# Performance work log

Hardware: AMD Instinct MI355X
Metric: run time of the kernel (lower is better)

## Reference

```python
import jax, jax.numpy as jnp
import numpy as np

NUM_HEADS = 8
NUM_POINTS = 4


def setup_inputs() -> dict:
    key = jax.random.key(0)
    bs, h, w = 2, 128, 128
    cin = cout = 256
    nq = h * w
    ks = jax.random.split(key, 6)
    query = jax.random.normal(ks[0], (bs, nq, cin), jnp.float32)
    value = jax.random.normal(ks[1], (bs, nq, cin), jnp.float32)
    # sampling_offsets: small random weight, bias = directional grid init (as in init_weights)
    W_off = jax.random.normal(ks[2], (cin, NUM_HEADS * NUM_POINTS * 2), jnp.float32) * 0.01
    thetas = np.arange(NUM_HEADS, dtype=np.float32) * (2.0 * np.pi / NUM_HEADS)
    grid = np.stack([np.cos(thetas), np.sin(thetas)], -1)
    grid = grid / np.abs(grid).max(-1, keepdims=True)
    grid = np.tile(grid[:, None, :], (1, NUM_POINTS, 1)) * (np.arange(NUM_POINTS, dtype=np.float32)[None, :, None] + 1.0)
    b_off = jnp.asarray(grid.reshape(-1), jnp.float32)
    W_attn = jax.random.normal(ks[3], (cin, NUM_HEADS * NUM_POINTS), jnp.float32) * 0.01
    b_attn = jnp.zeros((NUM_HEADS * NUM_POINTS,), jnp.float32)
    s = 1.0 / np.sqrt(cin)  # xavier-ish uniform
    W_val = jax.random.uniform(ks[4], (cin, cout), jnp.float32, -s, s)
    b_val = jnp.zeros((cout,), jnp.float32)
    W_out = jax.random.uniform(ks[5], (cout, cout), jnp.float32, -s, s)
    b_out = jnp.zeros((cout,), jnp.float32)
    return {"query": query, "value": value, "W_off": W_off, "b_off": b_off,
            "W_attn": W_attn, "b_attn": b_attn, "W_val": W_val, "b_val": b_val,
            "W_out": W_out, "b_out": b_out, "h": h, "w": w}


def _bilinear_sample(v_flat, ix, iy, h, w):
    # v_flat: (bs, heads, h*w, d); ix/iy: (bs, heads, nq, P) pixel coords.
    # grid_sample bilinear, align_corners=False, padding_mode='zeros'.
    x0 = jnp.floor(ix)
    y0 = jnp.floor(iy)
    wx1 = ix - x0
    wy1 = iy - y0
    bs, hd, nq, P = ix.shape
    acc = 0.0
    corners = ((x0, y0, (1.0 - wx1) * (1.0 - wy1)),
               (x0 + 1.0, y0, wx1 * (1.0 - wy1)),
               (x0, y0 + 1.0, (1.0 - wx1) * wy1),
               (x0 + 1.0, y0 + 1.0, wx1 * wy1))
    for xc, yc, wgt in corners:
        xi = xc.astype(jnp.int32)
        yi = yc.astype(jnp.int32)
        valid = (xi >= 0) & (xi < w) & (yi >= 0) & (yi < h)
        idx = jnp.clip(yi, 0, h - 1) * w + jnp.clip(xi, 0, w - 1)
        g = jnp.take_along_axis(v_flat, idx.reshape(bs, hd, nq * P)[..., None], axis=2)
        acc = acc + g.reshape(bs, hd, nq, P, -1) * (wgt * valid)[..., None]
    return acc  # (bs, heads, nq, P, d)


def deform_attn(query, value, W_off, b_off, W_attn, b_attn, W_val, b_val, h, w):
    bs, nq, _ = query.shape
    d = W_val.shape[1] // NUM_HEADS
    v = (value @ W_val + b_val).reshape(bs, nq, NUM_HEADS, d)
    off = (query @ W_off + b_off).reshape(bs, nq, NUM_HEADS, NUM_POINTS, 2)
    aw = jax.nn.softmax((query @ W_attn + b_attn).reshape(bs, nq, NUM_HEADS, NUM_POINTS), axis=-1)
    # reference points in [0,1], scale_ratio=1.0, (x, y) order
    ys = (jnp.arange(h, dtype=jnp.float32) + 0.5) / h
    xs = (jnp.arange(w, dtype=jnp.float32) + 0.5) / w
    ry, rx = jnp.meshgrid(ys, xs, indexing='ij')
    ref = jnp.stack([rx.reshape(-1), ry.reshape(-1)], -1)  # (nq, 2)
    loc = ref[None, :, None, None, :] + off / jnp.array([w, h], jnp.float32)
    grid = 2.0 * loc - 1.0  # normalized grid_sample coords
    grid = grid.transpose(0, 2, 1, 3, 4)  # (bs, heads, nq, P, 2)
    ix = (grid[..., 0] + 1.0) * (w / 2.0) - 0.5
    iy = (grid[..., 1] + 1.0) * (h / 2.0) - 0.5
    v_flat = v.transpose(0, 2, 1, 3)  # (bs, heads, h*w, d)
    sampled = _bilinear_sample(v_flat, ix, iy, h, w)  # (bs, heads, nq, P, d)
    out = (sampled * aw.transpose(0, 2, 1, 3)[..., None]).sum(3)  # (bs, heads, nq, d)
    return out.transpose(0, 2, 1, 3).reshape(bs, nq, NUM_HEADS * d)


def reference(query, value, W_off, b_off, W_attn, b_attn, W_val, b_val, W_out, b_out, h, w):
    attn = deform_attn(query, value, W_off, b_off, W_attn, b_attn, W_val, b_val, h, w)
    # dropout acts as identity in eval mode; identity residual = query
    return attn @ W_out + b_out + query
```

## Files before the change

### kernel.cpp

```cpp
#include <hip/hip_runtime.h>

#define H_IMG 128
#define W_IMG 128
#define NQ (H_IMG * W_IMG)
#define CIN 256
#define NH 8
#define NP 4
#define DH 32
#define LDSP 264

typedef __bf16 bf16x4 __attribute__((ext_vector_type(4)));
typedef __bf16 bf16x8 __attribute__((ext_vector_type(8)));
typedef _Float16 f16x8 __attribute__((ext_vector_type(8)));
typedef float f32x4 __attribute__((ext_vector_type(4)));

__global__ __launch_bounds__(256) void prep_weights(
    const float* __restrict__ Wval, const float* __restrict__ Wout,
    const float* __restrict__ Woff, const float* __restrict__ Wattn,
    const float* __restrict__ boff, const float* __restrict__ battn,
    __bf16* __restrict__ btv, _Float16* __restrict__ bto,
    __bf16* __restrict__ btoa, float* __restrict__ bias96) {
  int id = blockIdx.x * 256 + threadIdx.x;
  if (id < 256 * 256) {
    int n = id >> 8, k = id & 255;
    btv[n * 256 + k] = (__bf16)Wval[k * 256 + n];
    bto[n * 256 + k] = (_Float16)Wout[k * 256 + n];
  }
  if (id < 96 * 256) {
    int n = id >> 8, k = id & 255;
    float w = (n < 64) ? Woff[k * 64 + n] : Wattn[k * 32 + (n - 64)];
    btoa[n * 256 + k] = (__bf16)w;
  }
  if (id < 96) {
    bias96[id] = (id < 64) ? boff[id] : battn[id - 64];
  }
}

__global__ __launch_bounds__(512, 8) void gemm_v(
    const float* __restrict__ A, const __bf16* __restrict__ BT,
    const float* __restrict__ bias, _Float16* __restrict__ v, int M) {
  const int t = threadIdx.x;
  const int lane = t & 63;
  const int wave = t >> 6;
  const int r = lane & 15;
  const int q = lane >> 4;
  const int b = blockIdx.x;
  const int gm0 = (b & 511) * 64;
  const int wn = (b >> 9) * 128 + wave * 16;

  __shared__ __bf16 As[64 * LDSP];

#pragma unroll
  for (int i = 0; i < 8; ++i) {
    int g = i * 512 + t;
    int row = g >> 6, c4 = g & 63;
    float4 f = *(const float4*)(A + (size_t)(gm0 + row) * 256 + c4 * 4);
    bf16x4 hh;
    hh[0] = (__bf16)f.x; hh[1] = (__bf16)f.y;
    hh[2] = (__bf16)f.z; hh[3] = (__bf16)f.w;
    *(bf16x4*)(&As[row * LDSP + c4 * 4]) = hh;
  }
  __syncthreads();

  f32x4 acc[4];
#pragma unroll
  for (int mt = 0; mt < 4; ++mt) acc[mt] = (f32x4){0.f, 0.f, 0.f, 0.f};

#pragma unroll
  for (int kt = 0; kt < 8; ++kt) {
    const int ko = kt * 32 + q * 8;
    bf16x8 a[4];
#pragma unroll
    for (int mt = 0; mt < 4; ++mt)
      a[mt] = *(const bf16x8*)(&As[(mt * 16 + r) * LDSP + ko]);
    bf16x8 bb = *(const bf16x8*)(BT + (size_t)(wn + r) * 256 + ko);
#pragma unroll
    for (int mt = 0; mt < 4; ++mt)
      acc[mt] = __builtin_amdgcn_mfma_f32_16x16x32_bf16(a[mt], bb, acc[mt], 0, 0, 0);
  }

#pragma unroll
  for (int mt = 0; mt < 4; ++mt)
#pragma unroll
    for (int rr = 0; rr < 4; ++rr) {
      int row = gm0 + mt * 16 + q * 4 + rr;
      int col = wn + r;
      v[((size_t)(col >> 5) * M + row) * 32 + (col & 31)] =
          (_Float16)(acc[mt][rr] + bias[col]);
    }
}

__global__ __launch_bounds__(256, 2) void oa_sample_out(
    const float* __restrict__ query, const __bf16* __restrict__ btoa,
    const float* __restrict__ bias96, const _Float16* __restrict__ v,
    const _Float16* __restrict__ bto, const float* __restrict__ b_out,
    float* __restrict__ out, int M) {
  const int t = threadIdx.x;
  const int lane = t & 63;
  const int wave = t >> 6;
  const int r = lane & 15;
  const int q = lane >> 4;
  const int gm0 = blockIdx.x * 64;

  __shared__ __bf16 As[64 * LDSP];
  __shared__ float oas[64 * 100];
  _Float16* Asf = (_Float16*)As;

#pragma unroll
  for (int i = 0; i < 16; ++i) {
    int g = i * 256 + t;
    int row = g >> 6, c4 = g & 63;
    float4 f = *(const float4*)(query + (size_t)(gm0 + row) * 256 + c4 * 4);
    bf16x4 hh;
    hh[0] = (__bf16)f.x; hh[1] = (__bf16)f.y;
    hh[2] = (__bf16)f.z; hh[3] = (__bf16)f.w;
    *(bf16x4*)(&As[row * LDSP + c4 * 4]) = hh;
  }

  float resid[4][4][4];
#pragma unroll
  for (int mt = 0; mt < 4; ++mt)
#pragma unroll
    for (int nt = 0; nt < 4; ++nt)
#pragma unroll
      for (int rr = 0; rr < 4; ++rr)
        resid[mt][nt][rr] =
            query[(size_t)(gm0 + mt * 16 + q * 4 + rr) * 256 + wave * 64 + nt * 16 + r];

  __syncthreads();

  {
    const int wm = (wave & 1) * 32;
    const int n0 = (wave >> 1) * 48;
    f32x4 acc[2][3];
#pragma unroll
    for (int mt = 0; mt < 2; ++mt)
#pragma unroll
      for (int nt = 0; nt < 3; ++nt) acc[mt][nt] = (f32x4){0.f, 0.f, 0.f, 0.f};
#pragma unroll
    for (int kt = 0; kt < 8; ++kt) {
      const int ko = kt * 32 + q * 8;
      bf16x8 a0 = *(const bf16x8*)(&As[(wm + r) * LDSP + ko]);
      bf16x8 a1 = *(const bf16x8*)(&As[(wm + 16 + r) * LDSP + ko]);
      bf16x8 b[3];
#pragma unroll
      for (int nt = 0; nt < 3; ++nt)
        b[nt] = *(const bf16x8*)(btoa + (size_t)(n0 + nt * 16 + r) * 256 + ko);
#pragma unroll
      for (int nt = 0; nt < 3; ++nt) {
        acc[0][nt] = __builtin_amdgcn_mfma_f32_16x16x32_bf16(a0, b[nt], acc[0][nt], 0, 0, 0);
        acc[1][nt] = __builtin_amdgcn_mfma_f32_16x16x32_bf16(a1, b[nt], acc[1][nt], 0, 0, 0);
      }
    }
#pragma unroll
    for (int mt = 0; mt < 2; ++mt)
#pragma unroll
      for (int nt = 0; nt < 3; ++nt)
#pragma unroll
        for (int rr = 0; rr < 4; ++rr) {
          int rl = wm + mt * 16 + q * 4 + rr;
          int col = n0 + nt * 16 + r;
          oas[rl * 100 + col] = acc[mt][nt][rr] + bias96[col];
        }
  }
  __syncthreads();

  {
    const int qrow = t >> 2;
    const int c8 = (t & 3) * 8;
    const int row = gm0 + qrow;
    const int b = row >> 14;
    const int qi = row & (NQ - 1);
    const int x = qi & (W_IMG - 1);
    const int y = qi >> 7;
    const float* oar = &oas[qrow * 100];
#pragma unroll
    for (int h = 0; h < NH; ++h) {
      float l0 = oar[64 + h * 4 + 0];
      float l1 = oar[64 + h * 4 + 1];
      float l2 = oar[64 + h * 4 + 2];
      float l3 = oar[64 + h * 4 + 3];
      float mx = fmaxf(fmaxf(l0, l1), fmaxf(l2, l3));
      float e0 = __expf(l0 - mx), e1 = __expf(l1 - mx);
      float e2 = __expf(l2 - mx), e3 = __expf(l3 - mx);
      float inv = 1.f / (e0 + e1 + e2 + e3);
      float awp[4] = {e0 * inv, e1 * inv, e2 * inv, e3 * inv};

      int offs[16];
      float wvs[16];
#pragma unroll
      for (int p = 0; p < NP; ++p) {
        float ox = oar[h * 8 + p * 2 + 0];
        float oy = oar[h * 8 + p * 2 + 1];
        float ix = (float)x + ox;
        float iy = (float)y + oy;
        float x0f = floorf(ix), y0f = floorf(iy);
        float wx1 = ix - x0f, wy1 = iy - y0f;
        int x0 = (int)x0f, y0 = (int)y0f;
        float wgt[4] = {(1.f - wx1) * (1.f - wy1), wx1 * (1.f - wy1),
                        (1.f - wx1) * wy1, wx1 * wy1};
        int xs[4] = {x0, x0 + 1, x0, x0 + 1};
        int ysv[4] = {y0, y0, y0 + 1, y0 + 1};
#pragma unroll
        for (int c = 0; c < 4; ++c) {
          int xi = xs[c], yi = ysv[c];
          bool valid = (xi >= 0) & (xi < W_IMG) & (yi >= 0) & (yi < H_IMG);
          int xc = xi < 0 ? 0 : (xi > W_IMG - 1 ? W_IMG - 1 : xi);
          int yc = yi < 0 ? 0 : (yi > H_IMG - 1 ? H_IMG - 1 : yi);
          offs[p * 4 + c] = (yc * W_IMG + xc) * (DH * 2);
          wvs[p * 4 + c] = awp[p] * wgt[c] * (valid ? 1.f : 0.f);
        }
      }

      const char* vb =
          (const char*)v + ((size_t)h * M + (size_t)b * NQ) * (DH * 2) + c8 * 2;
      f16x8 g[16];
#pragma unroll
      for (int i = 0; i < 16; ++i) g[i] = *(const f16x8*)(vb + offs[i]);

      f16x8 fa = {};
#pragma unroll
      for (int i = 0; i < 16; ++i) fa += g[i] * (_Float16)wvs[i];

      *(f16x8*)(&Asf[qrow * LDSP + h * DH + c8]) = fa;
    }
  }
  __syncthreads();

  {
    const int wn = wave * 64;
    f32x4 acc[4][4];
#pragma unroll
    for (int mt = 0; mt < 4; ++mt)
#pragma unroll
      for (int nt = 0; nt < 4; ++nt) acc[mt][nt] = (f32x4){0.f, 0.f, 0.f, 0.f};
#pragma unroll
    for (int kt = 0; kt < 8; ++kt) {
      const int ko = kt * 32 + q * 8;
      f16x8 a[4], b[4];
#pragma unroll
      for (int mt = 0; mt < 4; ++mt)
        a[mt] = *(const f16x8*)(&Asf[(mt * 16 + r) * LDSP + ko]);
#pragma unroll
      for (int nt = 0; nt < 4; ++nt)
        b[nt] = *(const f16x8*)(bto + (size_t)(wn + nt * 16 + r) * 256 + ko);
#pragma unroll
      for (int mt = 0; mt < 4; ++mt)
#pragma unroll
        for (int nt = 0; nt < 4; ++nt)
          acc[mt][nt] =
              __builtin_amdgcn_mfma_f32_16x16x32_f16(a[mt], b[nt], acc[mt][nt], 0, 0, 0);
    }
#pragma unroll
    for (int mt = 0; mt < 4; ++mt)
#pragma unroll
      for (int nt = 0; nt < 4; ++nt)
#pragma unroll
        for (int rr = 0; rr < 4; ++rr) {
          int row = gm0 + mt * 16 + q * 4 + rr;
          int col = wn + nt * 16 + r;
          out[(size_t)row * 256 + col] =
              acc[mt][nt][rr] + b_out[col] + resid[mt][nt][rr];
        }
  }
}

extern "C" void kernel_launch(void* const* d_in, const int* in_sizes, int n_in,
                              void* d_out, int out_size, void* d_ws, size_t ws_size,
                              hipStream_t stream) {
  const float* query  = (const float*)d_in[0];
  const float* value  = (const float*)d_in[1];
  const float* W_off  = (const float*)d_in[2];
  const float* b_off  = (const float*)d_in[3];
  const float* W_attn = (const float*)d_in[4];
  const float* b_attn = (const float*)d_in[5];
  const float* W_val  = (const float*)d_in[6];
  const float* b_val  = (const float*)d_in[7];
  const float* W_out  = (const float*)d_in[8];
  const float* b_out  = (const float*)d_in[9];
  float* out = (float*)d_out;

  char* ws = (char*)d_ws;
  __bf16*   btv    = (__bf16*)(ws + 0);
  _Float16* bto    = (_Float16*)(ws + 131072);
  __bf16*   btoa   = (__bf16*)(ws + 262144);
  float*    bias96 = (float*)(ws + 311296);
  _Float16* v      = (_Float16*)(ws + 524288);

  const int M = in_sizes[0] / CIN;

  prep_weights<<<256, 256, 0, stream>>>(W_val, W_out, W_off, W_attn,
                                        b_off, b_attn, btv, bto, btoa, bias96);
  gemm_v<<<(M / 64) * 2, 512, 0, stream>>>(value, btv, b_val, v, M);
  oa_sample_out<<<M / 64, 256, 0, stream>>>(query, btoa, bias96, v, bto, b_out, out, M);
}
```

Baseline: 158.3 us.

## Halve query tile per block and remap blocks to XCDs for locality

The fused offset/attention, sampling and output-projection kernel now processes 32 queries per block instead of 64, doubling the grid size. In the sampling stage each thread handles 4 of the 8 heads, so the work stays spread across all 256 threads. Block indices are remapped so that the two halves of each former 64-row tile land on the same XCD, which should keep L2 reuse of nearby value rows. The change cuts LDS and register use per block and raises parallelism, at the cost of less weight reuse per block in both MFMA GEMMs.

```diff
diff --git a/kernel.cpp b/kernel.cpp
--- a/kernel.cpp
+++ b/kernel.cpp
@@ -8,6 +8,7 @@
 #define NP 4
 #define DH 32
 #define LDSP 264
+#define QB 32
 
 typedef __bf16 bf16x4 __attribute__((ext_vector_type(4)));
 typedef __bf16 bf16x8 __attribute__((ext_vector_type(8)));
@@ -100,14 +101,18 @@
   const int wave = t >> 6;
   const int r = lane & 15;
   const int q = lane >> 4;
-  const int gm0 = blockIdx.x * 64;
-
-  __shared__ __bf16 As[64 * LDSP];
-  __shared__ float oas[64 * 100];
+  const int c = blockIdx.x;
+  const int xcd = c & 7;
+  const int j = c >> 3;
+  const int P = xcd + 8 * (j >> 1);
+  const int gm0 = P * 64 + (j & 1) * 32;
+
+  __shared__ __bf16 As[QB * LDSP];
+  __shared__ float oas[QB * 100];
   _Float16* Asf = (_Float16*)As;
 
 #pragma unroll
-  for (int i = 0; i < 16; ++i) {
+  for (int i = 0; i < 8; ++i) {
     int g = i * 256 + t;
     int row = g >> 6, c4 = g & 63;
     float4 f = *(const float4*)(query + (size_t)(gm0 + row) * 256 + c4 * 4);
@@ -117,9 +122,9 @@
     *(bf16x4*)(&As[row * LDSP + c4 * 4]) = hh;
   }
 
-  float resid[4][4][4];
-#pragma unroll
-  for (int mt = 0; mt < 4; ++mt)
+  float resid[2][4][4];
+#pragma unroll
+  for (int mt = 0; mt < 2; ++mt)
 #pragma unroll
     for (int nt = 0; nt < 4; ++nt)
 #pragma unroll
@@ -130,43 +135,38 @@
   __syncthreads();
 
   {
-    const int wm = (wave & 1) * 32;
+    const int wm = (wave & 1) * 16;
     const int n0 = (wave >> 1) * 48;
-    f32x4 acc[2][3];
-#pragma unroll
-    for (int mt = 0; mt < 2; ++mt)
-#pragma unroll
-      for (int nt = 0; nt < 3; ++nt) acc[mt][nt] = (f32x4){0.f, 0.f, 0.f, 0.f};
+    f32x4 acc[3];
+#pragma unroll
+    for (int nt = 0; nt < 3; ++nt) acc[nt] = (f32x4){0.f, 0.f, 0.f, 0.f};
 #pragma unroll
     for (int kt = 0; kt < 8; ++kt) {
       const int ko = kt * 32 + q * 8;
-      bf16x8 a0 = *(const bf16x8*)(&As[(wm + r) * LDSP + ko]);
-      bf16x8 a1 = *(const bf16x8*)(&As[(wm + 16 + r) * LDSP + ko]);
+      bf16x8 a = *(const bf16x8*)(&As[(wm + r) * LDSP + ko]);
       bf16x8 b[3];
 #pragma unroll
       for (int nt = 0; nt < 3; ++nt)
         b[nt] = *(const bf16x8*)(btoa + (size_t)(n0 + nt * 16 + r) * 256 + ko);
 #pragma unroll
-      for (int nt = 0; nt < 3; ++nt) {
-        acc[0][nt] = __builtin_amdgcn_mfma_f32_16x16x32_bf16(a0, b[nt], acc[0][nt], 0, 0, 0);
-        acc[1][nt] = __builtin_amdgcn_mfma_f32_16x16x32_bf16(a1, b[nt], acc[1][nt], 0, 0, 0);
+      for (int nt = 0; nt < 3; ++nt)
+        acc[nt] = __builtin_amdgcn_mfma_f32_16x16x32_bf16(a, b[nt], acc[nt], 0, 0, 0);
+    }
+#pragma unroll
+    for (int nt = 0; nt < 3; ++nt)
+#pragma unroll
+      for (int rr = 0; rr < 4; ++rr) {
+        int rl = wm + q * 4 + rr;
+        int col = n0 + nt * 16 + r;
+        oas[rl * 100 + col] = acc[nt][rr] + bias96[col];
       }
-    }
-#pragma unroll
-    for (int mt = 0; mt < 2; ++mt)
-#pragma unroll
-      for (int nt = 0; nt < 3; ++nt)
-#pragma unroll
-        for (int rr = 0; rr < 4; ++rr) {
-          int rl = wm + mt * 16 + q * 4 + rr;
-          int col = n0 + nt * 16 + r;
-          oas[rl * 100 + col] = acc[mt][nt][rr] + bias96[col];
-        }
   }
   __syncthreads();
 
   {
-    const int qrow = t >> 2;
+    const int slot = t >> 2;
+    const int qrow = slot & (QB - 1);
+    const int hgrp = slot >> 5;
     const int c8 = (t & 3) * 8;
     const int row = gm0 + qrow;
     const int b = row >> 14;
@@ -175,7 +175,8 @@
     const int y = qi >> 7;
     const float* oar = &oas[qrow * 100];
 #pragma unroll
-    for (int h = 0; h < NH; ++h) {
+    for (int hh_ = 0; hh_ < 4; ++hh_) {
+      const int h = hgrp * 4 + hh_;
       float l0 = oar[64 + h * 4 + 0];
       float l1 = oar[64 + h * 4 + 1];
       float l2 = oar[64 + h * 4 + 2];
@@ -202,13 +203,13 @@
         int xs[4] = {x0, x0 + 1, x0, x0 + 1};
         int ysv[4] = {y0, y0, y0 + 1, y0 + 1};
 #pragma unroll
-        for (int c = 0; c < 4; ++c) {
-          int xi = xs[c], yi = ysv[c];
+        for (int cc = 0; cc < 4; ++cc) {
+          int xi = xs[cc], yi = ysv[cc];
           bool valid = (xi >= 0) & (xi < W_IMG) & (yi >= 0) & (yi < H_IMG);
           int xc = xi < 0 ? 0 : (xi > W_IMG - 1 ? W_IMG - 1 : xi);
           int yc = yi < 0 ? 0 : (yi > H_IMG - 1 ? H_IMG - 1 : yi);
-          offs[p * 4 + c] = (yc * W_IMG + xc) * (DH * 2);
-          wvs[p * 4 + c] = awp[p] * wgt[c] * (valid ? 1.f : 0.f);
+          offs[p * 4 + cc] = (yc * W_IMG + xc) * (DH * 2);
+          wvs[p * 4 + cc] = awp[p] * wgt[cc] * (valid ? 1.f : 0.f);
         }
       }
 
@@ -229,30 +230,30 @@
 
   {
     const int wn = wave * 64;
-    f32x4 acc[4][4];
-#pragma unroll
-    for (int mt = 0; mt < 4; ++mt)
+    f32x4 acc[2][4];
+#pragma unroll
+    for (int mt = 0; mt < 2; ++mt)
 #pragma unroll
       for (int nt = 0; nt < 4; ++nt) acc[mt][nt] = (f32x4){0.f, 0.f, 0.f, 0.f};
 #pragma unroll
     for (int kt = 0; kt < 8; ++kt) {
       const int ko = kt * 32 + q * 8;
-      f16x8 a[4], b[4];
-#pragma unroll
-      for (int mt = 0; mt < 4; ++mt)
+      f16x8 a[2], b[4];
+#pragma unroll
+      for (int mt = 0; mt < 2; ++mt)
         a[mt] = *(const f16x8*)(&Asf[(mt * 16 + r) * LDSP + ko]);
 #pragma unroll
       for (int nt = 0; nt < 4; ++nt)
         b[nt] = *(const f16x8*)(bto + (size_t)(wn + nt * 16 + r) * 256 + ko);
 #pragma unroll
-      for (int mt = 0; mt < 4; ++mt)
+      for (int mt = 0; mt < 2; ++mt)
 #pragma unroll
         for (int nt = 0; nt < 4; ++nt)
           acc[mt][nt] =
               __builtin_amdgcn_mfma_f32_16x16x32_f16(a[mt], b[nt], acc[mt][nt], 0, 0, 0);
     }
 #pragma unroll
-    for (int mt = 0; mt < 4; ++mt)
+    for (int mt = 0; mt < 2; ++mt)
 #pragma unroll
       for (int nt = 0; nt < 4; ++nt)
 #pragma unroll
@@ -292,5 +293,5 @@
   prep_weights<<<256, 256, 0, stream>>>(W_val, W_out, W_off, W_attn,
                                         b_off, b_attn, btv, bto, btoa, bias96);
   gemm_v<<<(M / 64) * 2, 512, 0, stream>>>(value, btv, b_val, v, M);
-  oa_sample_out<<<M / 64, 256, 0, stream>>>(query, btoa, bias96, v, bto, b_out, out, M);
-}
+  oa_sample_out<<<M / QB, 256, 0, stream>>>(query, btoa, bias96, v, bto, b_out, out, M);
+}
```

New measurement: 168.5 us. 1.06x slower.
